# Performance work log

Hardware: AMD Instinct MI355X
Metric: run time of the kernel (lower is better)

Reference implementation:

```python
import jax, jax.numpy as jnp
import numpy as np

HEADS = 4

def _layernorm(x, g, b, eps=1e-5):
    mu = x.mean(-1, keepdims=True)
    var = ((x - mu) ** 2).mean(-1, keepdims=True)
    return (x - mu) / jnp.sqrt(var + eps) * g + b

def _feature_map(data, proj, is_query, eps=1e-4):
    # FAVOR+ softmax kernel features. data: [B,H,S,dh], proj: [m,dh]
    dh = data.shape[-1]
    m = proj.shape[0]
    dn = dh ** -0.25
    ratio = m ** -0.5
    dash = jnp.einsum('bhsd,md->bhsm', data * dn, proj)
    diag = 0.5 * jnp.sum((data * dn) ** 2, axis=-1, keepdims=True)
    mx = jnp.max(dash, axis=-1, keepdims=True) if is_query else jnp.max(dash)
    return ratio * (jnp.exp(dash - diag - mx) + eps)

def _causal_linear_attention(q, k, v):
    # q,k: [B,H,S,m] kernel features; v: [B,H,S,dh]
    k_cum = jnp.cumsum(k, axis=2)                                  # [B,H,S,m]
    d_inv = 1.0 / jnp.einsum('bhsm,bhsm->bhs', q, k_cum)           # [B,H,S]
    ctx = jnp.cumsum(jnp.einsum('bhsm,bhsd->bhsmd', k, v), axis=2) # [B,H,S,m,dh]
    return jnp.einsum('bhsmd,bhsm,bhs->bhsd', ctx, q, d_inv)

def reference(x, pre_w, pre_b, ln1_g, ln1_b, wq, wk, wv, wo, bo, proj,
              ln2_g, ln2_b, ff_w1, ff_b1, ff_w2, ff_b2, tgt_w, tgt_b, rd_w, rd_b):
    # preproc: 1x1x1 conv3d + softplus
    xbn = jax.nn.softplus(jnp.einsum('bcthw,oc->bothw', x, pre_w)
                          + pre_b[None, :, None, None, None])
    B, D, T, H, W = xbn.shape
    tokens = xbn.reshape(B, -1, D)  # raw torch-style reshape, S = T*H*W
    S = tokens.shape[1]

    # Performer block (depth=1): prenorm attention + prenorm FF, residuals
    h = _layernorm(tokens, ln1_g, ln1_b)
    split = lambda t: t.reshape(B, S, HEADS, -1).transpose(0, 2, 1, 3)
    q, k, v = split(h @ wq), split(h @ wk), split(h @ wv)
    qp = _feature_map(q, proj, True)
    kp = _feature_map(k, proj, False)
    attn = _causal_linear_attention(qp, kp, v)
    attn = attn.transpose(0, 2, 1, 3).reshape(B, S, D)
    tokens = tokens + attn @ wo + bo
    h2 = _layernorm(tokens, ln2_g, ln2_b)
    tokens = tokens + jax.nn.gelu(h2 @ ff_w1 + ff_b1, approximate=False) @ ff_w2 + ff_b2

    # readout
    out = tokens.reshape(B, D, T, H, W).mean(axis=2)               # [B,D,H,W]
    out = jnp.concatenate([out, x[:, 2, 0][:, None]], axis=1)      # [B,D+1,H,W]
    out = jax.lax.conv_general_dilated(out, tgt_w, (1, 1), [(2, 2), (2, 2)],
                                       dimension_numbers=('NCHW', 'OIHW', 'NCHW'))
    out = out + tgt_b[None, :, None, None]
    out = out.mean(axis=(2, 3))                                    # global avg pool -> [B,1]
    return out @ rd_w.T + rd_b


def setup_inputs() -> dict:
    key = jax.random.key(0)
    ks = jax.random.split(key, 12)
    B, T, H, W = 2, 8, 48, 48
    D, DH, M, FF = 64, 16, 32, 256
    s = lambda k, shape, sc=1.0: jax.random.normal(k, shape, jnp.float32) * sc
    inv = 1.0 / np.sqrt(D)
    return {
        'x': s(ks[0], (B, 3, T, H, W)),
        'pre_w': s(ks[1], (D, 3), 1.0 / np.sqrt(3)),
        'pre_b': jnp.zeros((D,), jnp.float32),
        'ln1_g': jnp.ones((D,), jnp.float32), 'ln1_b': jnp.zeros((D,), jnp.float32),
        'wq': s(ks[2], (D, D), inv), 'wk': s(ks[3], (D, D), inv), 'wv': s(ks[4], (D, D), inv),
        'wo': s(ks[5], (D, D), inv), 'bo': jnp.zeros((D,), jnp.float32),
        'proj': s(ks[6], (M, DH)),
        'ln2_g': jnp.ones((D,), jnp.float32), 'ln2_b': jnp.zeros((D,), jnp.float32),
        'ff_w1': s(ks[7], (D, FF), inv), 'ff_b1': jnp.zeros((FF,), jnp.float32),
        'ff_w2': s(ks[8], (FF, D), 1.0 / np.sqrt(FF)), 'ff_b2': jnp.zeros((D,), jnp.float32),
        'tgt_w': s(ks[9], (1, D + 1, 5, 5), 1.0 / np.sqrt((D + 1) * 25)),
        'tgt_b': jnp.zeros((1,), jnp.float32),
        'rd_w': s(ks[10], (1, 1)), 'rd_b': jnp.zeros((1,), jnp.float32),
    }
```

## Files before the change

kernel.cpp:

```cpp
#include <hip/hip_runtime.h>
#include <hip/hip_bf16.h>
#include <math.h>

typedef __hip_bfloat16 bf16;
typedef __attribute__((ext_vector_type(8))) short short8;
typedef __attribute__((ext_vector_type(16))) float floatx16;

constexpr int B_   = 2;
constexpr int T_   = 8;
constexpr int HW   = 48 * 48;
constexpr int S_   = T_ * HW;
constexpr int D_   = 64;
constexpr int NH   = 4;
constexpr int DH   = 16;
constexpr int M_   = 32;
constexpr int BS   = B_ * S_;
constexpr int BSD  = BS * D_;
constexpr int BH   = B_ * NH;
constexpr int BHS  = BH * S_;
constexpr int CHUNK = 32;
constexpr int NC   = S_ / CHUNK;
constexpr int STATE = M_ * DH + M_;
constexpr int GSLOTS = 64;
constexpr int GSTRIDE = 32;
constexpr int SCB = 16;
constexpr int SRG = 16;
constexpr int SRUN = NC / SRG;
constexpr float DN = 0.5f;
constexpr float RATIO = 0.17677669529663687f;

__device__ __forceinline__ unsigned short f2bf(float f) {
  bf16 h = __float2bfloat16(f);
  return *reinterpret_cast<unsigned short*>(&h);
}
__device__ __forceinline__ float bf2f(bf16 v) { return __bfloat162float(v); }
__device__ __forceinline__ float bfs2f(short s) {
  return __uint_as_float(((unsigned)(unsigned short)s) << 16);
}
__device__ __forceinline__ void atomicMaxFloat(float* addr, float val) {
  if (val >= 0.f) atomicMax((int*)addr, __float_as_int(val));
  else atomicMin((unsigned int*)addr, __float_as_uint(val));
}

__global__ void __launch_bounds__(256) k_prep(const float* __restrict__ wq,
        const float* __restrict__ wk, const float* __restrict__ wv,
        const float* __restrict__ wo, const float* __restrict__ w1,
        const float* __restrict__ proj,
        short* __restrict__ wqT, short* __restrict__ wkT, short* __restrict__ wvT,
        short* __restrict__ woT, short* __restrict__ w1T, short* __restrict__ projb,
        float* __restrict__ gmax) {
  int tid = blockIdx.x * 256 + threadIdx.x;
  if (tid < GSLOTS) ((unsigned*)gmax)[tid * GSTRIDE] = 0xff800000u;
  if (tid < 512) projb[tid] = (short)f2bf(proj[tid]);
  if (tid < 4096) {
    int c = tid >> 6, r = tid & 63;
    wqT[tid] = (short)f2bf(wq[r * 64 + c]);
    wkT[tid] = (short)f2bf(wk[r * 64 + c]);
    wvT[tid] = (short)f2bf(wv[r * 64 + c]);
    woT[tid] = (short)f2bf(wo[r * 64 + c]);
  }
  {
    int c = tid >> 6, r = tid & 63;
    w1T[tid] = (short)f2bf(w1[r * 256 + c]);
  }
}

__global__ void __launch_bounds__(256) k_preqkv(const float* __restrict__ x,
                      const float* __restrict__ pw, const float* __restrict__ pb,
                      const float* __restrict__ g, const float* __restrict__ bb,
                      const short* __restrict__ wqT, const short* __restrict__ wkT,
                      const short* __restrict__ wvT, const short* __restrict__ projb,
                      bf16* __restrict__ tok, bf16* __restrict__ q,
                      bf16* __restrict__ k, bf16* __restrict__ v,
                      float* __restrict__ gmax) {
  __shared__ __align__(16) short sh[32 * 64];
  __shared__ __align__(16) short sk[32 * 64];
  int tid = threadIdx.x;
  int tbase = blockIdx.x * 32;

  {
    size_t f0 = (size_t)tbase * 64;
    int b = (int)(f0 / ((size_t)D_ * S_));
    int rem = (int)(f0 % ((size_t)D_ * S_));
    int d = rem / S_;
    int pos0 = rem % S_;
    float w0 = pw[d * 3 + 0], w1 = pw[d * 3 + 1], w2 = pw[d * 3 + 2], pbd = pb[d];
    const float* xb = x + ((size_t)b * 3) * S_ + pos0 + tid * 8;
    float4 x0a = *(const float4*)(xb);
    float4 x0b = *(const float4*)(xb + 4);
    float4 x1a = *(const float4*)(xb + S_);
    float4 x1b = *(const float4*)(xb + S_ + 4);
    float4 x2a = *(const float4*)(xb + 2 * S_);
    float4 x2b = *(const float4*)(xb + 2 * S_ + 4);
    float xf0[8] = {x0a.x, x0a.y, x0a.z, x0a.w, x0b.x, x0b.y, x0b.z, x0b.w};
    float xf1[8] = {x1a.x, x1a.y, x1a.z, x1a.w, x1b.x, x1b.y, x1b.z, x1b.w};
    float xf2[8] = {x2a.x, x2a.y, x2a.z, x2a.w, x2b.x, x2b.y, x2b.z, x2b.w};
    float t[8];
    short8 tv;
#pragma unroll
    for (int j = 0; j < 8; ++j) {
      float a = xf0[j] * w0 + xf1[j] * w1 + xf2[j] * w2 + pbd;
      t[j] = fmaxf(a, 0.f) + log1pf(expf(-fabsf(a)));
      tv[j] = (short)f2bf(t[j]);
    }
    *(short8*)(tok + f0 + (size_t)tid * 8) = tv;
    float s1 = 0.f, s2 = 0.f;
#pragma unroll
    for (int j = 0; j < 8; ++j) { s1 += t[j]; s2 += t[j] * t[j]; }
#pragma unroll
    for (int off = 4; off; off >>= 1) {
      s1 += __shfl_xor(s1, off, 8);
      s2 += __shfl_xor(s2, off, 8);
    }
    float mu = s1 * (1.f / 64.f);
    float var = s2 * (1.f / 64.f) - mu * mu;
    float rs = rsqrtf(var + 1e-5f);
    int tt = tid >> 3, j8 = tid & 7;
    short8 hv;
#pragma unroll
    for (int j = 0; j < 8; ++j) {
      int c = j8 * 8 + j;
      hv[j] = (short)f2bf((t[j] - mu) * rs * g[c] + bb[c]);
    }
    *(short8*)&sh[tt * 64 + ((j8 ^ (tt & 7)) * 8)] = hv;
  }
  __syncthreads();

  int w = tid >> 6;
  int L = tid & 63;
  int half = L >> 5;
  int n = L & 31;

  if (w < 3) {
    const short* wmT = (w == 0) ? wqT : (w == 1) ? wkT : wvT;
    bf16* outm = (w == 0) ? q : (w == 1) ? k : v;

    short8 a[4];
#pragma unroll
    for (int c = 0; c < 4; ++c)
      a[c] = *(const short8*)&sh[n * 64 + (((c * 2 + half) ^ (n & 7)) * 8)];
#pragma unroll
    for (int ct = 0; ct < 2; ++ct) {
      int col = ct * 32 + n;
      short8 bfrag[4];
#pragma unroll
      for (int c = 0; c < 4; ++c)
        bfrag[c] = *(const short8*)&wmT[col * 64 + c * 16 + half * 8];
      floatx16 acc;
#pragma unroll
      for (int i = 0; i < 16; ++i) acc[i] = 0.f;
      acc = __builtin_amdgcn_mfma_f32_32x32x16_bf16(a[0], bfrag[0], acc, 0, 0, 0);
      acc = __builtin_amdgcn_mfma_f32_32x32x16_bf16(a[1], bfrag[1], acc, 0, 0, 0);
      acc = __builtin_amdgcn_mfma_f32_32x32x16_bf16(a[2], bfrag[2], acc, 0, 0, 0);
      acc = __builtin_amdgcn_mfma_f32_32x32x16_bf16(a[3], bfrag[3], acc, 0, 0, 0);
      int head = col >> 4, di = col & 15;
#pragma unroll
      for (int r = 0; r < 16; ++r) {
        int row = (r & 3) + 8 * (r >> 2) + 4 * half;
        int token = tbase + row;
        int b = token / S_, s = token % S_;
        unsigned short us = f2bf(acc[r]);
        if (w == 2) {
          outm[((size_t)(b * NH + head) * S_ + s) * DH + di] = *(bf16*)&us;
        } else {
          unsigned short usd = f2bf(bfs2f((short)us) * DN);
          outm[((size_t)(b * NH + head) * S_ + s) * DH + di] = *(bf16*)&usd;
          if (w == 1)
            *(short*)((char*)sk + row * 128 + ((col * 2) ^ ((row & 7) << 4))) = (short)usd;
        }
      }
    }
  }
  __syncthreads();

  {
    short8 ak;
    short8 bp = *(const short8*)&projb[n * 16 + half * 8];
    int roff = n * 128 + ((w * 32 + half * 16) ^ ((n & 7) << 4));
    ak = *(const short8*)((const char*)sk + roff);
    floatx16 Pk;
#pragma unroll
    for (int i = 0; i < 16; ++i) Pk[i] = 0.f;
    Pk = __builtin_amdgcn_mfma_f32_32x32x16_bf16(ak, bp, Pk, 0, 0, 0);
    float bmax = -3.4e38f;
#pragma unroll
    for (int r = 0; r < 16; ++r) bmax = fmaxf(bmax, Pk[r]);
    for (int off = 32; off; off >>= 1) bmax = fmaxf(bmax, __shfl_xor(bmax, off));
    if (L == 0)
      atomicMaxFloat(&gmax[((blockIdx.x * 4 + w) & (GSLOTS - 1)) * GSTRIDE], bmax);
  }
}

__global__ void __launch_bounds__(256) k_featcsfin(const float* __restrict__ gmax,
                      const bf16* __restrict__ q, const bf16* __restrict__ k,
                      const bf16* __restrict__ v, const short* __restrict__ projb,
                      bf16* __restrict__ qpb, bf16* __restrict__ kpb,
                      float* __restrict__ ckv) {
  __shared__ __align__(16) float sKp[4][CHUNK * 32];
  int tid = threadIdx.x;
  int w = tid >> 6, L = tid & 63, half = L >> 5, n = L & 31;
  short8 bp = *(const short8*)&projb[n * 16 + half * 8];

  if (blockIdx.x >= BH * NC / 4) {
    int fblk = blockIdx.x - BH * NC / 4;
    int rowbase = fblk * 128 + w * 32;
    short8 aq = *(const short8*)(q + (size_t)(rowbase + n) * 16 + half * 8);
    float dq = 0.f;
#pragma unroll
    for (int j = 0; j < 8; ++j) { float f = bfs2f(aq[j]); dq += f * f; }
    dq += __shfl_xor(dq, 32);
    dq *= 0.5f;
    floatx16 Pq;
#pragma unroll
    for (int i = 0; i < 16; ++i) Pq[i] = 0.f;
    Pq = __builtin_amdgcn_mfma_f32_32x32x16_bf16(aq, bp, Pq, 0, 0, 0);
#pragma unroll
    for (int r = 0; r < 16; ++r) {
      int i = (r & 3) + 8 * (r >> 2) + 4 * half;
      float mx = Pq[r];
      for (int off = 16; off; off >>= 1) mx = fmaxf(mx, __shfl_xor(mx, off, 32));
      float dqi = __shfl(dq, i, 64);
      float val = RATIO * (expf(Pq[r] - dqi - mx) + 1e-4f);
      qpb[(size_t)(rowbase + i) * 32 + n] = __float2bfloat16(val);
    }
    return;
  }

  int chunk = blockIdx.x * 4 + w;
  int bh = chunk / NC, c = chunk % NC;
  int base = bh * S_ + c * CHUNK;
  float gm = gmax[L * GSTRIDE];
  for (int off = 32; off; off >>= 1) gm = fmaxf(gm, __shfl_xor(gm, off));
  short8 ak = *(const short8*)(k + (size_t)(base + n) * 16 + half * 8);
  float dk = 0.f;
#pragma unroll
  for (int j = 0; j < 8; ++j) { float f = bfs2f(ak[j]); dk += f * f; }
  dk += __shfl_xor(dk, 32);
  dk *= 0.5f;
  floatx16 Pk;
#pragma unroll
  for (int i = 0; i < 16; ++i) Pk[i] = 0.f;
  Pk = __builtin_amdgcn_mfma_f32_32x32x16_bf16(ak, bp, Pk, 0, 0, 0);
  float* sp = &sKp[w][0];
#pragma unroll
  for (int r = 0; r < 16; ++r) {
    int i = (r & 3) + 8 * (r >> 2) + 4 * half;
    float dgi = __shfl(dk, i, 64);
    sp[i * 32 + n] = RATIO * (expf(Pk[r] - dgi - gm) + 1e-4f);
  }
  short8 a1, a2;
#pragma unroll
  for (int j = 0; j < 8; ++j) {
    a1[j] = (short)f2bf(sp[(half * 8 + j) * 32 + n]);
    a2[j] = (short)f2bf(sp[(16 + half * 8 + j) * 32 + n]);
  }
  const unsigned short one_bf = f2bf(1.f);
  short8 vb1, vb2;
#pragma unroll
  for (int j = 0; j < 8; ++j) {
    int t1 = half * 8 + j, t2 = 16 + half * 8 + j;
    vb1[j] = (n < 16) ? *(const short*)(v + (size_t)(base + t1) * 16 + n)
                      : (short)(n == 16 ? one_bf : 0);
    vb2[j] = (n < 16) ? *(const short*)(v + (size_t)(base + t2) * 16 + n)
                      : (short)(n == 16 ? one_bf : 0);
  }
  floatx16 O;
#pragma unroll
  for (int i = 0; i < 16; ++i) O[i] = 0.f;
  O = __builtin_amdgcn_mfma_f32_32x32x16_bf16(a1, vb1, O, 0, 0, 0);
  O = __builtin_amdgcn_mfma_f32_32x32x16_bf16(a2, vb2, O, 0, 0, 0);
  float* outp = ckv + (size_t)chunk * STATE;
#pragma unroll
  for (int r = 0; r < 16; ++r) {
    int m = (r & 3) + 8 * (r >> 2) + 4 * half;
    if (n < 16) outp[m * 16 + n] = O[r];
    else if (n == 16) outp[512 + m] = O[r];
  }
  {
    int row = L >> 1, c8 = (L & 1) * 16;
    const float* srcp = sp + row * 32 + c8;
    uint4 u0, u1;
    u0.x = (unsigned)f2bf(srcp[0])  | ((unsigned)f2bf(srcp[1])  << 16);
    u0.y = (unsigned)f2bf(srcp[2])  | ((unsigned)f2bf(srcp[3])  << 16);
    u0.z = (unsigned)f2bf(srcp[4])  | ((unsigned)f2bf(srcp[5])  << 16);
    u0.w = (unsigned)f2bf(srcp[6])  | ((unsigned)f2bf(srcp[7])  << 16);
    u1.x = (unsigned)f2bf(srcp[8])  | ((unsigned)f2bf(srcp[9])  << 16);
    u1.y = (unsigned)f2bf(srcp[10]) | ((unsigned)f2bf(srcp[11]) << 16);
    u1.z = (unsigned)f2bf(srcp[12]) | ((unsigned)f2bf(srcp[13]) << 16);
    u1.w = (unsigned)f2bf(srcp[14]) | ((unsigned)f2bf(srcp[15]) << 16);
    *(uint4*)&kpb[(size_t)(base + row) * 32 + c8] = u0;
    *(uint4*)&kpb[(size_t)(base + row) * 32 + c8 + 8] = u1;
  }
}

__global__ void __launch_bounds__(256) k_scan(float* __restrict__ ckv) {
  __shared__ float sS[SRG][SCB];
  int blk = blockIdx.x;
  int bh = blk / (STATE / SCB);
  int c0 = (blk % (STATE / SCB)) * SCB;
  int cl = threadIdx.x & (SCB - 1);
  int rg = threadIdx.x >> 4;
  int c = c0 + cl;
  size_t base = ((size_t)bh * NC + rg * SRUN) * STATE + c;
  float s = 0.f;
#pragma unroll 6
  for (int i = 0; i < SRUN; ++i) s += ckv[base + (size_t)i * STATE];
  sS[rg][cl] = s;
  __syncthreads();
  float run = 0.f;
  for (int r = 0; r < rg; ++r) run += sS[r][cl];
  for (int i0 = 0; i0 < SRUN; i0 += 6) {
    float tb[6];
#pragma unroll
    for (int j = 0; j < 6; ++j) tb[j] = ckv[base + (size_t)(i0 + j) * STATE];
#pragma unroll
    for (int j = 0; j < 6; ++j) {
      ckv[base + (size_t)(i0 + j) * STATE] = run;
      run += tb[j];
    }
  }
}

__global__ void __launch_bounds__(256) k_attn(const bf16* __restrict__ qpb,
                                              const bf16* __restrict__ kpb,
                                              const bf16* __restrict__ v,
                                              const float* __restrict__ ckv,
                                              bf16* __restrict__ attn) {
  __shared__ __align__(16) float sP[4][32 * 33 + 4];
  int tid = threadIdx.x;
  int w = tid >> 6;
  int L = tid & 63;
  int half = L >> 5;
  int n = L & 31;
  int chunk = blockIdx.x * 4 + w;
  int bh = chunk / NC, c = chunk % NC;
  int base = bh * S_ + c * CHUNK;

  short8 a1 = *(const short8*)(qpb + (size_t)(base + n) * 32 + half * 8);
  short8 a2 = *(const short8*)(qpb + (size_t)(base + n) * 32 + 16 + half * 8);
  short8 b1 = *(const short8*)(kpb + (size_t)(base + n) * 32 + half * 8);
  short8 b2 = *(const short8*)(kpb + (size_t)(base + n) * 32 + 16 + half * 8);

  floatx16 P;
#pragma unroll
  for (int i = 0; i < 16; ++i) P[i] = 0.f;
  P = __builtin_amdgcn_mfma_f32_32x32x16_bf16(a1, b1, P, 0, 0, 0);
  P = __builtin_amdgcn_mfma_f32_32x32x16_bf16(a2, b2, P, 0, 0, 0);

  float* sp = &sP[w][0];
#pragma unroll
  for (int r = 0; r < 16; ++r) {
    int i = (r & 3) + 8 * (r >> 2) + 4 * half;
    sp[i * 33 + n] = (n <= i) ? P[r] : 0.f;
  }
  __syncthreads();
  short8 pa1, pa2;
#pragma unroll
  for (int j = 0; j < 8; ++j) {
    pa1[j] = (short)f2bf(sp[n * 33 + half * 8 + j]);
    pa2[j] = (short)f2bf(sp[n * 33 + 16 + half * 8 + j]);
  }

  const float* cs = ckv + (size_t)chunk * STATE;
  const unsigned short one_bf = f2bf(1.f);
  short8 vb1, vb2, sb1, sb2;
#pragma unroll
  for (int j = 0; j < 8; ++j) {
    int t1 = half * 8 + j, t2 = 16 + half * 8 + j;
    vb1[j] = (n < 16) ? *(const short*)(v + (size_t)(base + t1) * 16 + n)
                      : (short)(n == 16 ? one_bf : 0);
    vb2[j] = (n < 16) ? *(const short*)(v + (size_t)(base + t2) * 16 + n)
                      : (short)(n == 16 ? one_bf : 0);
    float y1 = (n < 16) ? cs[t1 * 16 + n] : (n == 16 ? cs[512 + t1] : 0.f);
    float y2 = (n < 16) ? cs[t2 * 16 + n] : (n == 16 ? cs[512 + t2] : 0.f);
    sb1[j] = (short)f2bf(y1);
    sb2[j] = (short)f2bf(y2);
  }

  floatx16 O;
#pragma unroll
  for (int i = 0; i < 16; ++i) O[i] = 0.f;
  O = __builtin_amdgcn_mfma_f32_32x32x16_bf16(pa1, vb1, O, 0, 0, 0);
  O = __builtin_amdgcn_mfma_f32_32x32x16_bf16(pa2, vb2, O, 0, 0, 0);
  O = __builtin_amdgcn_mfma_f32_32x32x16_bf16(a1, sb1, O, 0, 0, 0);
  O = __builtin_amdgcn_mfma_f32_32x32x16_bf16(a2, sb2, O, 0, 0, 0);

  int srcl = 16 + 32 * half;
  float res[16];
#pragma unroll
  for (int r = 0; r < 16; ++r) {
    float den = __shfl(O[r], srcl, 64);
    res[r] = O[r] / den;
  }
  if (n < 16) {
    int b = bh >> 2, head = bh & 3;
#pragma unroll
    for (int r = 0; r < 16; ++r) {
      int i = (r & 3) + 8 * (r >> 2) + 4 * half;
      attn[((size_t)(b * S_ + c * CHUNK + i)) * 64 + head * 16 + n] = __float2bfloat16(res[r]);
    }
  }
}

__global__ void __launch_bounds__(128) k_wo_ln(const bf16* __restrict__ attn,
                        const short* __restrict__ woT, const float* __restrict__ bo,
                        const bf16* __restrict__ tok, const float* __restrict__ g,
                        const float* __restrict__ bb,
                        bf16* __restrict__ tok2, bf16* __restrict__ h2) {
  __shared__ __align__(16) float sC[32 * 68];
  int tid = threadIdx.x;
  int w = tid >> 6;
  int L = tid & 63;
  int half = L >> 5;
  int n = L & 31;
  int tbase = blockIdx.x * 32;

  short8 a[4];
  {
    const bf16* arow = attn + (size_t)(tbase + n) * 64 + half * 8;
#pragma unroll
    for (int c = 0; c < 4; ++c) a[c] = *(const short8*)(arow + c * 16);
  }
  int col = w * 32 + n;
  short8 bfrag[4];
#pragma unroll
  for (int c = 0; c < 4; ++c)
    bfrag[c] = *(const short8*)&woT[col * 64 + c * 16 + half * 8];
  floatx16 acc;
#pragma unroll
  for (int i = 0; i < 16; ++i) acc[i] = 0.f;
  acc = __builtin_amdgcn_mfma_f32_32x32x16_bf16(a[0], bfrag[0], acc, 0, 0, 0);
  acc = __builtin_amdgcn_mfma_f32_32x32x16_bf16(a[1], bfrag[1], acc, 0, 0, 0);
  acc = __builtin_amdgcn_mfma_f32_32x32x16_bf16(a[2], bfrag[2], acc, 0, 0, 0);
  acc = __builtin_amdgcn_mfma_f32_32x32x16_bf16(a[3], bfrag[3], acc, 0, 0, 0);
  float bias = bo[col];
#pragma unroll
  for (int r = 0; r < 16; ++r) {
    int row = (r & 3) + 8 * (r >> 2) + 4 * half;
    sC[row * 68 + col] = acc[r] + bf2f(tok[(size_t)(tbase + row) * 64 + col]) + bias;
  }
  __syncthreads();
  int tg = tid >> 5, cg = tid & 31;
  int c0 = cg * 2, c1 = c0 + 1;
  float g0 = g[c0], g1 = g[c1], be0 = bb[c0], be1 = bb[c1];
#pragma unroll
  for (int i = 0; i < 8; ++i) {
    int lrow = tg * 8 + i;
    int token = tbase + lrow;
    float t0 = sC[lrow * 68 + c0];
    float t1 = sC[lrow * 68 + c1];
    float s1 = t0 + t1, s2 = t0 * t0 + t1 * t1;
    for (int off = 16; off; off >>= 1) {
      s1 += __shfl_xor(s1, off, 32);
      s2 += __shfl_xor(s2, off, 32);
    }
    float mu = s1 * (1.f / 64.f);
    float var = s2 * (1.f / 64.f) - mu * mu;
    float rs = rsqrtf(var + 1e-5f);
    tok2[token * 64 + c0] = __float2bfloat16(t0);
    tok2[token * 64 + c1] = __float2bfloat16(t1);
    h2[token * 64 + c0] = __float2bfloat16((t0 - mu) * rs * g0 + be0);
    h2[token * 64 + c1] = __float2bfloat16((t1 - mu) * rs * g1 + be1);
  }
}

__global__ void __launch_bounds__(256) k_ffg(const bf16* __restrict__ h2,
                                             const short* __restrict__ w1T,
                                             const float* __restrict__ b1,
                                             float* __restrict__ Gavg) {
  int tid = threadIdx.x;
  int w = tid >> 6;
  int L = tid & 63;
  int half = L >> 5;
  int n = L & 31;
  int blk = blockIdx.x;
  int b = blk / 576;
  int rem = blk % 576;
  int ch = rem / 9;
  int jp0 = (rem % 9) * 4;
  int token_n = b * 18432 + ch * 288 + (n & 7) * 36 + jp0 + (n >> 3);

  short8 a[4];
  {
    const bf16* hrow = h2 + (size_t)token_n * 64 + half * 8;
#pragma unroll
    for (int c = 0; c < 4; ++c) a[c] = *(const short8*)(hrow + c * 16);
  }
  size_t gbase = ((size_t)(b * 64 + ch) * 36 + jp0);
#pragma unroll
  for (int ct = 0; ct < 2; ++ct) {
    int col = w * 64 + ct * 32 + n;
    short8 bfrag[4];
#pragma unroll
    for (int c = 0; c < 4; ++c)
      bfrag[c] = *(const short8*)&w1T[col * 64 + c * 16 + half * 8];
    floatx16 acc;
#pragma unroll
    for (int i = 0; i < 16; ++i) acc[i] = 0.f;
    acc = __builtin_amdgcn_mfma_f32_32x32x16_bf16(a[0], bfrag[0], acc, 0, 0, 0);
    acc = __builtin_amdgcn_mfma_f32_32x32x16_bf16(a[1], bfrag[1], acc, 0, 0, 0);
    acc = __builtin_amdgcn_mfma_f32_32x32x16_bf16(a[2], bfrag[2], acc, 0, 0, 0);
    acc = __builtin_amdgcn_mfma_f32_32x32x16_bf16(a[3], bfrag[3], acc, 0, 0, 0);
    float bias = b1[col];
#pragma unroll
    for (int j = 0; j < 4; ++j) {
      float s = 0.f;
#pragma unroll
      for (int rr = 0; rr < 4; ++rr) {
        float xg = acc[j * 4 + rr] + bias;
        s += 0.5f * xg * (1.f + erff(xg * 0.70710678118654752f));
      }
      s += __shfl_xor(s, 32);
      if (half == 0)
        Gavg[(gbase + j) * 256 + col] = s * 0.125f;
    }
  }
}

__global__ void __launch_bounds__(256) k_pool2(const float* __restrict__ Gavg,
                        const bf16* __restrict__ tok2, const float* __restrict__ w2,
                        const float* __restrict__ b2, float* __restrict__ pool) {
  __shared__ __align__(16) float sG[18 * 256];
  __shared__ __align__(16) float sRed[4 * 18 * 64];
  int blk = blockIdx.x;
  int b = blk / 128;
  int rem = blk % 128;
  int ch = rem >> 1, jph = rem & 1;
  int tid = threadIdx.x;
  size_t grow0 = ((size_t)(b * 64 + ch) * 36 + jph * 18) * 256;
  for (int e = tid; e < 1152; e += 256) {
    int row = e >> 6, c4 = e & 63;
    *(float4*)&sG[row * 256 + c4 * 4] = *(const float4*)&Gavg[grow0 + row * 256 + c4 * 4];
  }
  __syncthreads();
  int kg = tid >> 6, dd = tid & 63;
  float acc[18];
#pragma unroll
  for (int i = 0; i < 18; ++i) acc[i] = 0.f;
  for (int k4 = 0; k4 < 16; ++k4) {
    int k = kg * 64 + k4 * 4;
    float w0 = w2[(k + 0) * 64 + dd];
    float w1 = w2[(k + 1) * 64 + dd];
    float w2v = w2[(k + 2) * 64 + dd];
    float w3 = w2[(k + 3) * 64 + dd];
#pragma unroll
    for (int i = 0; i < 18; ++i) {
      float4 gf = *(const float4*)&sG[i * 256 + k];
      acc[i] += gf.x * w0 + gf.y * w1 + gf.z * w2v + gf.w * w3;
    }
  }
#pragma unroll
  for (int i = 0; i < 18; ++i) sRed[(kg * 18 + i) * 64 + dd] = acc[i];
  __syncthreads();
  for (int o = tid; o < 1152; o += 256) {
    int jp18 = o >> 6, d2 = o & 63;
    float gsum = sRed[(0 * 18 + jp18) * 64 + d2] + sRed[(1 * 18 + jp18) * 64 + d2]
               + sRed[(2 * 18 + jp18) * 64 + d2] + sRed[(3 * 18 + jp18) * 64 + d2];
    int p = (jph * 18 + jp18) * 64 + d2;
    size_t tbase = (size_t)b * 1179648 + (size_t)ch * 18432 + p;
    float ts = 0.f;
#pragma unroll
    for (int t = 0; t < 8; ++t) ts += bf2f(tok2[tbase + t * 2304]);
    pool[((size_t)(b * 64 + ch)) * HW + p] = ts * 0.125f + gsum + b2[d2];
  }
}

__global__ void __launch_bounds__(256) k_convsum(const float* __restrict__ pool,
                                                 const float* __restrict__ x,
                                                 const float* __restrict__ w,
                                                 float* __restrict__ partial) {
  int blk = blockIdx.x;
  int b = blk / 65, ch = blk % 65;
  int tid = threadIdx.x;
  __shared__ float cls[25];
  __shared__ float red[256];
  if (tid < 25) {
    int ry = tid / 5, rx = tid % 5;
    int kh0 = (ry <= 2) ? 0 : (ry == 3 ? 1 : 2);
    int kh1 = (ry >= 2) ? 4 : (ry == 1 ? 3 : 2);
    int kw0 = (rx <= 2) ? 0 : (rx == 3 ? 1 : 2);
    int kw1 = (rx >= 2) ? 4 : (rx == 1 ? 3 : 2);
    float s = 0.f;
    for (int kh = kh0; kh <= kh1; ++kh)
      for (int kw = kw0; kw <= kw1; ++kw)
        s += w[ch * 25 + kh * 5 + kw];
    cls[tid] = s;
  }
  __syncthreads();
  const float* pc = (ch < 64) ? (pool + ((size_t)(b * 64 + ch)) * HW)
                              : (x + (size_t)b * 3 * S_ + 2 * S_);
  float acc = 0.f;
#pragma unroll
  for (int e = tid; e < HW; e += 256) {
    int iy = e / 48, ix = e % 48;
    int ry = (iy == 0) ? 0 : (iy == 1) ? 1 : (iy <= 45) ? 2 : (iy == 46) ? 3 : 4;
    int rx = (ix == 0) ? 0 : (ix == 1) ? 1 : (ix <= 45) ? 2 : (ix == 46) ? 3 : 4;
    acc += pc[e] * cls[ry * 5 + rx];
  }
  red[tid] = acc;
  __syncthreads();
  for (int s = 128; s; s >>= 1) {
    if (tid < s) red[tid] += red[tid + s];
    __syncthreads();
  }
  if (!tid) partial[blk] = red[0];
}

__global__ void k_final(const float* __restrict__ partial, const float* __restrict__ tgt_b,
                        const float* __restrict__ rd_w, const float* __restrict__ rd_b,
                        float* __restrict__ out) {
  int b = blockIdx.x;
  int lane = threadIdx.x;
  float s = (lane < 65) ? partial[b * 65 + lane] : 0.f;
  for (int off = 32; off; off >>= 1) s += __shfl_down(s, off, 64);
  __shared__ float r2;
  if (lane == 64) r2 = s;
  __syncthreads();
  if (!lane) {
    float tot = s + r2;
    float mean = tot / 2304.f + tgt_b[0];
    out[b] = mean * rd_w[0] + rd_b[0];
  }
}

extern "C" void kernel_launch(void* const* d_in, const int* in_sizes, int n_in,
                              void* d_out, int out_size, void* d_ws, size_t ws_size,
                              hipStream_t stream) {
  const float* x     = (const float*)d_in[0];
  const float* pre_w = (const float*)d_in[1];
  const float* pre_b = (const float*)d_in[2];
  const float* ln1_g = (const float*)d_in[3];
  const float* ln1_b = (const float*)d_in[4];
  const float* wq    = (const float*)d_in[5];
  const float* wk    = (const float*)d_in[6];
  const float* wv    = (const float*)d_in[7];
  const float* wo    = (const float*)d_in[8];
  const float* bo    = (const float*)d_in[9];
  const float* proj  = (const float*)d_in[10];
  const float* ln2_g = (const float*)d_in[11];
  const float* ln2_b = (const float*)d_in[12];
  const float* ff_w1 = (const float*)d_in[13];
  const float* ff_b1 = (const float*)d_in[14];
  const float* ff_w2 = (const float*)d_in[15];
  const float* ff_b2 = (const float*)d_in[16];
  const float* tgt_w = (const float*)d_in[17];
  const float* tgt_b = (const float*)d_in[18];
  const float* rd_w  = (const float*)d_in[19];
  const float* rd_b  = (const float*)d_in[20];
  float* out = (float*)d_out;

  float* ws = (float*)d_ws;
  bf16*  tok   = (bf16*)ws;
  bf16*  v     = (bf16*)(ws + (size_t)BSD);
  bf16*  q     = (bf16*)(ws + 2 * (size_t)BSD);
  float* Gavg  = ws + 2 * (size_t)BSD;
  float* pool  = Gavg + 1179648;
  bf16*  k     = (bf16*)(ws + 3 * (size_t)BSD);
  bf16*  h2    = (bf16*)(ws + 4 * (size_t)BSD);
  bf16*  qpb   = (bf16*)(ws + 6 * (size_t)BSD);
  bf16*  kpb   = (bf16*)(ws + 7 * (size_t)BSD);
  float* ckv   = ws + 8 * (size_t)BSD;
  bf16*  tok2  = (bf16*)(ws + 8 * (size_t)BSD);
  bf16*  attnb = k;
  float* smalls = ws + 9 * (size_t)BSD + 147456;
  float* gmax  = smalls;
  float* partial = smalls + 2048;
  short* wqT   = (short*)(smalls + 2304);
  short* wkT   = (short*)(smalls + 4352);
  short* wvT   = (short*)(smalls + 6400);
  short* woT   = (short*)(smalls + 8448);
  short* w1T   = (short*)(smalls + 10496);
  short* projb = (short*)(smalls + 18688);

  k_prep<<<dim3(64), dim3(256), 0, stream>>>(wq, wk, wv, wo, ff_w1, proj,
                                             wqT, wkT, wvT, woT, w1T, projb, gmax);
  k_preqkv<<<dim3(BS / 32), dim3(256), 0, stream>>>(x, pre_w, pre_b, ln1_g, ln1_b,
                                                    wqT, wkT, wvT, projb, tok, q, k, v, gmax);
  k_featcsfin<<<dim3(BH * NC / 4 + BHS / 128), dim3(256), 0, stream>>>(gmax, q, k, v, projb,
                                                                       qpb, kpb, ckv);
  k_scan<<<dim3(BH * (STATE / SCB)), dim3(256), 0, stream>>>(ckv);
  k_attn<<<dim3(BH * NC / 4), dim3(256), 0, stream>>>(qpb, kpb, v, ckv, attnb);
  k_wo_ln<<<dim3(BS / 32), dim3(128), 0, stream>>>(attnb, woT, bo, tok, ln2_g, ln2_b, tok2, h2);
  k_ffg<<<dim3(B_ * 64 * 9), dim3(256), 0, stream>>>(h2, w1T, ff_b1, Gavg);
  k_pool2<<<dim3(B_ * 64 * 2), dim3(256), 0, stream>>>(Gavg, tok2, ff_w2, ff_b2, pool);
  k_convsum<<<dim3(B_ * 65), dim3(256), 0, stream>>>(pool, x, tgt_w, partial);
  k_final<<<dim3(B_), dim3(128), 0, stream>>>(partial, tgt_b, rd_w, rd_b, out);
}
```

Before: 195.3 us.

## Fuse pooling with conv-sum readout and reshape scan into more row groups

The pooling kernel now applies the 5x5-conv class weights directly and reduces to per-block partials, which removes the pooled-map write/read and the separate convsum kernel. The final kernel handles the extra x channel and sums the partials. Separately, the scan kernel uses 64 row groups of 4 columns and holds each run in registers, avoiding a second global read. This cuts one launch and some memory traffic. In exchange, the scan blocks are narrower and make strided accesses.

```diff
diff --git a/kernel.cpp b/kernel.cpp
--- a/kernel.cpp
+++ b/kernel.cpp
@@ -23,9 +23,9 @@
 constexpr int STATE = M_ * DH + M_;
 constexpr int GSLOTS = 64;
 constexpr int GSTRIDE = 32;
-constexpr int SCB = 16;
-constexpr int SRG = 16;
+constexpr int SRG = 64;
 constexpr int SRUN = NC / SRG;
+constexpr int SCB = 4;
 constexpr float DN = 0.5f;
 constexpr float RATIO = 0.17677669529663687f;
 
@@ -297,27 +297,25 @@
   __shared__ float sS[SRG][SCB];
   int blk = blockIdx.x;
   int bh = blk / (STATE / SCB);
-  int c0 = (blk % (STATE / SCB)) * SCB;
   int cl = threadIdx.x & (SCB - 1);
-  int rg = threadIdx.x >> 4;
-  int c = c0 + cl;
+  int rg = threadIdx.x >> 2;
+  int c = (blk % (STATE / SCB)) * SCB + cl;
   size_t base = ((size_t)bh * NC + rg * SRUN) * STATE + c;
+  float tb[SRUN];
   float s = 0.f;
-#pragma unroll 6
-  for (int i = 0; i < SRUN; ++i) s += ckv[base + (size_t)i * STATE];
+#pragma unroll
+  for (int i = 0; i < SRUN; ++i) {
+    tb[i] = ckv[base + (size_t)i * STATE];
+    s += tb[i];
+  }
   sS[rg][cl] = s;
   __syncthreads();
   float run = 0.f;
   for (int r = 0; r < rg; ++r) run += sS[r][cl];
-  for (int i0 = 0; i0 < SRUN; i0 += 6) {
-    float tb[6];
-#pragma unroll
-    for (int j = 0; j < 6; ++j) tb[j] = ckv[base + (size_t)(i0 + j) * STATE];
-#pragma unroll
-    for (int j = 0; j < 6; ++j) {
-      ckv[base + (size_t)(i0 + j) * STATE] = run;
-      run += tb[j];
-    }
+#pragma unroll
+  for (int i = 0; i < SRUN; ++i) {
+    ckv[base + (size_t)i * STATE] = run;
+    run += tb[i];
   }
 }
 
@@ -517,16 +515,31 @@
   }
 }
 
-__global__ void __launch_bounds__(256) k_pool2(const float* __restrict__ Gavg,
+__global__ void __launch_bounds__(256) k_poolgv(const float* __restrict__ Gavg,
                         const bf16* __restrict__ tok2, const float* __restrict__ w2,
-                        const float* __restrict__ b2, float* __restrict__ pool) {
+                        const float* __restrict__ b2, const float* __restrict__ wc,
+                        float* __restrict__ partial) {
   __shared__ __align__(16) float sG[18 * 256];
   __shared__ __align__(16) float sRed[4 * 18 * 64];
+  __shared__ float cls[25];
+  __shared__ float red[256];
   int blk = blockIdx.x;
   int b = blk / 128;
   int rem = blk % 128;
   int ch = rem >> 1, jph = rem & 1;
   int tid = threadIdx.x;
+  if (tid < 25) {
+    int ry = tid / 5, rx = tid % 5;
+    int kh0 = (ry <= 2) ? 0 : (ry == 3 ? 1 : 2);
+    int kh1 = (ry >= 2) ? 4 : (ry == 1 ? 3 : 2);
+    int kw0 = (rx <= 2) ? 0 : (rx == 3 ? 1 : 2);
+    int kw1 = (rx >= 2) ? 4 : (rx == 1 ? 3 : 2);
+    float s = 0.f;
+    for (int kh = kh0; kh <= kh1; ++kh)
+      for (int kw = kw0; kw <= kw1; ++kw)
+        s += wc[ch * 25 + kh * 5 + kw];
+    cls[tid] = s;
+  }
   size_t grow0 = ((size_t)(b * 64 + ch) * 36 + jph * 18) * 256;
   for (int e = tid; e < 1152; e += 256) {
     int row = e >> 6, c4 = e & 63;
@@ -552,6 +565,7 @@
 #pragma unroll
   for (int i = 0; i < 18; ++i) sRed[(kg * 18 + i) * 64 + dd] = acc[i];
   __syncthreads();
+  float csum = 0.f;
   for (int o = tid; o < 1152; o += 256) {
     int jp18 = o >> 6, d2 = o & 63;
     float gsum = sRed[(0 * 18 + jp18) * 64 + d2] + sRed[(1 * 18 + jp18) * 64 + d2]
@@ -561,16 +575,27 @@
     float ts = 0.f;
 #pragma unroll
     for (int t = 0; t < 8; ++t) ts += bf2f(tok2[tbase + t * 2304]);
-    pool[((size_t)(b * 64 + ch)) * HW + p] = ts * 0.125f + gsum + b2[d2];
-  }
-}
-
-__global__ void __launch_bounds__(256) k_convsum(const float* __restrict__ pool,
-                                                 const float* __restrict__ x,
-                                                 const float* __restrict__ w,
-                                                 float* __restrict__ partial) {
-  int blk = blockIdx.x;
-  int b = blk / 65, ch = blk % 65;
+    float pv = ts * 0.125f + gsum + b2[d2];
+    int iy = p / 48, ix = p % 48;
+    int ry = (iy == 0) ? 0 : (iy == 1) ? 1 : (iy <= 45) ? 2 : (iy == 46) ? 3 : 4;
+    int rx = (ix == 0) ? 0 : (ix == 1) ? 1 : (ix <= 45) ? 2 : (ix == 46) ? 3 : 4;
+    csum += pv * cls[ry * 5 + rx];
+  }
+  red[tid] = csum;
+  __syncthreads();
+  for (int s = 128; s; s >>= 1) {
+    if (tid < s) red[tid] += red[tid + s];
+    __syncthreads();
+  }
+  if (!tid) partial[blk] = red[0];
+}
+
+__global__ void __launch_bounds__(256) k_final(const float* __restrict__ partial,
+                        const float* __restrict__ x, const float* __restrict__ wc,
+                        const float* __restrict__ tgt_b,
+                        const float* __restrict__ rd_w, const float* __restrict__ rd_b,
+                        float* __restrict__ out) {
+  int b = blockIdx.x;
   int tid = threadIdx.x;
   __shared__ float cls[25];
   __shared__ float red[256];
@@ -583,12 +608,11 @@
     float s = 0.f;
     for (int kh = kh0; kh <= kh1; ++kh)
       for (int kw = kw0; kw <= kw1; ++kw)
-        s += w[ch * 25 + kh * 5 + kw];
+        s += wc[64 * 25 + kh * 5 + kw];
     cls[tid] = s;
   }
   __syncthreads();
-  const float* pc = (ch < 64) ? (pool + ((size_t)(b * 64 + ch)) * HW)
-                              : (x + (size_t)b * 3 * S_ + 2 * S_);
+  const float* pc = x + (size_t)b * 3 * S_ + 2 * S_;
   float acc = 0.f;
 #pragma unroll
   for (int e = tid; e < HW; e += 256) {
@@ -597,28 +621,15 @@
     int rx = (ix == 0) ? 0 : (ix == 1) ? 1 : (ix <= 45) ? 2 : (ix == 46) ? 3 : 4;
     acc += pc[e] * cls[ry * 5 + rx];
   }
+  if (tid < 128) acc += partial[b * 128 + tid];
   red[tid] = acc;
   __syncthreads();
   for (int s = 128; s; s >>= 1) {
     if (tid < s) red[tid] += red[tid + s];
     __syncthreads();
   }
-  if (!tid) partial[blk] = red[0];
-}
-
-__global__ void k_final(const float* __restrict__ partial, const float* __restrict__ tgt_b,
-                        const float* __restrict__ rd_w, const float* __restrict__ rd_b,
-                        float* __restrict__ out) {
-  int b = blockIdx.x;
-  int lane = threadIdx.x;
-  float s = (lane < 65) ? partial[b * 65 + lane] : 0.f;
-  for (int off = 32; off; off >>= 1) s += __shfl_down(s, off, 64);
-  __shared__ float r2;
-  if (lane == 64) r2 = s;
-  __syncthreads();
-  if (!lane) {
-    float tot = s + r2;
-    float mean = tot / 2304.f + tgt_b[0];
+  if (!tid) {
+    float mean = red[0] / 2304.f + tgt_b[0];
     out[b] = mean * rd_w[0] + rd_b[0];
   }
 }
@@ -654,7 +665,6 @@
   bf16*  v     = (bf16*)(ws + (size_t)BSD);
   bf16*  q     = (bf16*)(ws + 2 * (size_t)BSD);
   float* Gavg  = ws + 2 * (size_t)BSD;
-  float* pool  = Gavg + 1179648;
   bf16*  k     = (bf16*)(ws + 3 * (size_t)BSD);
   bf16*  h2    = (bf16*)(ws + 4 * (size_t)BSD);
   bf16*  qpb   = (bf16*)(ws + 6 * (size_t)BSD);
@@ -682,7 +692,6 @@
   k_attn<<<dim3(BH * NC / 4), dim3(256), 0, stream>>>(qpb, kpb, v, ckv, attnb);
   k_wo_ln<<<dim3(BS / 32), dim3(128), 0, stream>>>(attnb, woT, bo, tok, ln2_g, ln2_b, tok2, h2);
   k_ffg<<<dim3(B_ * 64 * 9), dim3(256), 0, stream>>>(h2, w1T, ff_b1, Gavg);
-  k_pool2<<<dim3(B_ * 64 * 2), dim3(256), 0, stream>>>(Gavg, tok2, ff_w2, ff_b2, pool);
-  k_convsum<<<dim3(B_ * 65), dim3(256), 0, stream>>>(pool, x, tgt_w, partial);
-  k_final<<<dim3(B_), dim3(128), 0, stream>>>(partial, tgt_b, rd_w, rd_b, out);
-}
+  k_poolgv<<<dim3(B_ * 128), dim3(256), 0, stream>>>(Gavg, tok2, ff_w2, ff_b2, tgt_w, partial);
+  k_final<<<dim3(B_), dim3(256), 0, stream>>>(partial, x, tgt_w, tgt_b, rd_w, rd_b, out);
+}
```

After: 212.4 us. +8.8%, slower.
